# Kernel optimization log

Hardware: AMD Instinct MI355X
Metric: run time of the kernel (lower is better)

Reference implementation:

```python
import jax, jax.numpy as jnp
import numpy as np

N = 4096
HIDDEN = 256
NUM_HEADS = 8
HEAD_DIM = HIDDEN // NUM_HEADS
LN_EPS = 1e-3


def setup_inputs() -> dict:
    key = jax.random.key(0)
    ks = jax.random.split(key, 8)
    s = 1.0 / np.sqrt(HIDDEN)
    feat = jax.random.normal(ks[0], (N, HIDDEN), dtype=jnp.float32)
    Wq = jax.random.normal(ks[1], (HIDDEN, HIDDEN), dtype=jnp.float32) * s
    bq = jnp.zeros((HIDDEN,), dtype=jnp.float32)
    Wkv = jax.random.normal(ks[2], (HIDDEN, 2 * HIDDEN), dtype=jnp.float32) * s
    bkv = jnp.zeros((2 * HIDDEN,), dtype=jnp.float32)
    Weg = jax.random.normal(ks[3], (HIDDEN, 2 * NUM_HEADS), dtype=jnp.float32) * s
    beg = jnp.zeros((2 * NUM_HEADS,), dtype=jnp.float32)
    ln_g = jnp.ones((HIDDEN,), dtype=jnp.float32)
    ln_b = jnp.zeros((HIDDEN,), dtype=jnp.float32)
    return {"feat": feat, "Wq": Wq, "bq": bq, "Wkv": Wkv, "bkv": bkv,
            "Weg": Weg, "beg": beg, "ln_g": ln_g, "ln_b": ln_b}


def reference(feat, Wq, bq, Wkv, bkv, Weg, beg, ln_g, ln_b):
    n = feat.shape[0]
    # projections
    Q = feat @ Wq + bq                                  # [N, hidden]
    KV = feat @ Wkv + bkv                               # [N, 2*hidden]
    K, V = jnp.split(KV, 2, axis=-1)
    EG = feat @ Weg + beg                               # [N, 2*heads]
    E, G = jnp.split(EG, 2, axis=-1)                    # each [N, heads]
    # reshape to [N, head_dim, heads] (heads is the FAST axis, as in torch .view)
    Q = Q.reshape(n, HEAD_DIM, NUM_HEADS) * (HEAD_DIM ** -0.5)
    K = K.reshape(n, HEAD_DIM, NUM_HEADS)
    V = V.reshape(n, HEAD_DIM, NUM_HEADS)
    # all-pairs scores with per-j edge bias: [N, N, heads]
    H = jnp.einsum('idh,jdh->ijh', Q, K) + E[None, :, :]
    # softmax over i (axis 0), post-softmax sigmoid gate (per j, h)
    A = jax.nn.softmax(H, axis=0) * jax.nn.sigmoid(G)[None, :, :]
    Va = jnp.einsum('ijh,jdh->idh', A, V).reshape(n, HIDDEN)
    # layernorm eps=1e-3
    mu = jnp.mean(Va, axis=-1, keepdims=True)
    var = jnp.var(Va, axis=-1, keepdims=True)
    return (Va - mu) * jax.lax.rsqrt(var + LN_EPS) * ln_g + ln_b
```

## Files before the change

### kernel.cpp

```cpp
#include <hip/hip_runtime.h>
#include <hip/hip_bf16.h>

#define N 4096
#define HID 256
#define NH 8
#define HD 32
#define NC 784
#define CH 8
#define JSPAN (N / CH)

typedef __attribute__((ext_vector_type(8))) short short8;
typedef __attribute__((ext_vector_type(4))) short short4v;
typedef __attribute__((ext_vector_type(4))) float f32x4;
typedef __attribute__((ext_vector_type(2))) unsigned int uint2v;
typedef __attribute__((ext_vector_type(4))) unsigned int uint4v;

#define QSCALE 0.25503482f

static __device__ __forceinline__ unsigned short f2bf(float f) {
    union { float f; unsigned u; } v; v.f = f;
    unsigned r = v.u + 0x7fff + ((v.u >> 16) & 1);
    return (unsigned short)(r >> 16);
}
static __device__ __forceinline__ float bf2f(unsigned short u) {
    union { unsigned u; float f; } v; v.u = ((unsigned)u) << 16; return v.f;
}
static __device__ __forceinline__ unsigned packbf2(float a, float b) {
    __hip_bfloat162 t = __float22bfloat162_rn(make_float2(a, b));
    unsigned u; __builtin_memcpy(&u, &t, 4); return u;
}

__global__ void k_prep(const float* __restrict__ feat, const float* __restrict__ Wq,
                       const float* __restrict__ Wkv, const float* __restrict__ Weg,
                       const float* __restrict__ bq, const float* __restrict__ bkv,
                       const float* __restrict__ beg, unsigned short* __restrict__ featb,
                       unsigned short* __restrict__ WbT, float* __restrict__ bC,
                       float* __restrict__ colS) {
    int bx = blockIdx.x;
    if (bx < 1024) {
        int t = bx * 256 + threadIdx.x;
        float4 v = ((const float4*)feat)[t];
        short4v o;
        o[0] = (short)f2bf(v.x); o[1] = (short)f2bf(v.y);
        o[2] = (short)f2bf(v.z); o[3] = (short)f2bf(v.w);
        ((short4v*)featb)[t] = o;
    } else {
        int c = bx - 1024, k = threadIdx.x;
        float w, b;
        if (c < 256)      { w = Wq[k * 256 + c];          b = bq[c]; }
        else if (c < 768) { w = Wkv[k * 512 + (c - 256)]; b = bkv[c - 256]; }
        else              { w = Weg[k * 16 + (c - 768)];  b = beg[c - 768]; }
        WbT[c * 256 + k] = f2bf(w);
        if (k == 0) bC[c] = b;
        if (c < 128) colS[c * 256 + k] = 0.f;
    }
}

__global__ __launch_bounds__(256) void k_proj(const unsigned short* __restrict__ featb,
                                              const unsigned short* __restrict__ WbT,
                                              const float* __restrict__ bC,
                                              unsigned short* __restrict__ Qp,
                                              unsigned short* __restrict__ Kp,
                                              unsigned short* __restrict__ VpT,
                                              float* __restrict__ sigG) {
    int w = threadIdx.x >> 6, l = threadIdx.x & 63;
    int il = l & 15, g = l >> 4;
    int c0 = blockIdx.x * 16;
    int i0 = (blockIdx.y * 4 + w) * 16;
    const short8* Arow = (const short8*)(featb + (size_t)(i0 + il) * HID);
    const short8* Brow = (const short8*)(WbT + (size_t)(c0 + il) * HID);
    f32x4 acc = {0.f, 0.f, 0.f, 0.f};
#pragma unroll
    for (int k0 = 0; k0 < HID; k0 += 32) {
        short8 a = Arow[(k0 >> 3) + g];
        short8 b = Brow[(k0 >> 3) + g];
        acc = __builtin_amdgcn_mfma_f32_16x16x32_bf16(a, b, acc, 0, 0, 0);
    }
    int c = c0 + il;
    float bias = bC[c];
#pragma unroll
    for (int r = 0; r < 4; ++r) {
        int i = i0 + g * 4 + r;
        float val = acc[r] + bias;
        if (c < 256) {
            int h = c & 7, d = c >> 3;
            Qp[((size_t)h * N + i) * HD + d] = f2bf(val * QSCALE);
        } else if (c < 512) {
            int cc = c - 256, h = cc & 7, d = cc >> 3;
            Kp[((size_t)h * N + i) * HD + d] = f2bf(val);
        } else if (c < 768) {
            int cc = c - 512, h = cc & 7, d = cc >> 3;
            VpT[((size_t)h * HD + d) * N + i] = f2bf(val);
        } else {
            int cc = c - 768;
            if (cc >= 8) sigG[(size_t)(cc - 8) * N + i] = 1.f / (1.f + __expf(-val));
        }
    }
}

__global__ __launch_bounds__(256) void k_pass1(const unsigned short* __restrict__ Qp,
                                               const unsigned short* __restrict__ Kp,
                                               float* __restrict__ colS) {
    int w = threadIdx.x >> 6, l = threadIdx.x & 63;
    int il = l & 15, g = l >> 4;
    int h = blockIdx.y;
    int j0 = (blockIdx.x * 4 + w) * 64;
    const unsigned short* Kh = Kp + (size_t)h * N * HD;
    short8 Kf[4];
#pragma unroll
    for (int t = 0; t < 4; ++t)
        Kf[t] = *(const short8*)(Kh + (size_t)(j0 + 16 * t + il) * HD + g * 8);
    const unsigned short* Qh = Qp + (size_t)h * N * HD;
    f32x4 z = {0.f, 0.f, 0.f, 0.f};
    float s[4] = {0.f, 0.f, 0.f, 0.f};
    int ibeg = blockIdx.z * 512;
    short8 Qa = *(const short8*)(Qh + (size_t)(ibeg + il) * HD + g * 8);
    short8 Qb = *(const short8*)(Qh + (size_t)(ibeg + 16 + il) * HD + g * 8);
    for (int i0 = ibeg; i0 < ibeg + 512; i0 += 32) {
        short8 cQa = Qa, cQb = Qb;
        int in = i0 + 32;
        Qa = *(const short8*)(Qh + (size_t)(in + il) * HD + g * 8);
        Qb = *(const short8*)(Qh + (size_t)(in + 16 + il) * HD + g * 8);
#pragma unroll
        for (int t = 0; t < 4; ++t) {
            f32x4 Sa = __builtin_amdgcn_mfma_f32_16x16x32_bf16(cQa, Kf[t], z, 0, 0, 0);
            f32x4 Sb = __builtin_amdgcn_mfma_f32_16x16x32_bf16(cQb, Kf[t], z, 0, 0, 0);
            s[t] += ((__builtin_amdgcn_exp2f(Sa[0]) + __builtin_amdgcn_exp2f(Sa[1]))
                   + (__builtin_amdgcn_exp2f(Sa[2]) + __builtin_amdgcn_exp2f(Sa[3])))
                  + ((__builtin_amdgcn_exp2f(Sb[0]) + __builtin_amdgcn_exp2f(Sb[1]))
                   + (__builtin_amdgcn_exp2f(Sb[2]) + __builtin_amdgcn_exp2f(Sb[3])));
        }
    }
#pragma unroll
    for (int t = 0; t < 4; ++t) {
        s[t] += __shfl_xor(s[t], 16);
        s[t] += __shfl_xor(s[t], 32);
    }
    if (g == 0) {
#pragma unroll
        for (int t = 0; t < 4; ++t)
            atomicAdd(&colS[(size_t)h * N + j0 + 16 * t + il], s[t]);
    }
}

__global__ void k_vprep(unsigned short* __restrict__ VpT,
                        const float* __restrict__ sigG,
                        const float* __restrict__ colS) {
    int row = blockIdx.x >> 1;
    int j0 = ((blockIdx.x & 1) * 256 + threadIdx.x) * 8;
    int h = row >> 5;
    unsigned short* p = VpT + (size_t)row * N + j0;
    short8 v = *(short8*)p;
    const float* sg = sigG + (size_t)h * N + j0;
    const float* cs = colS + (size_t)h * N + j0;
    f32x4 sa = *(const f32x4*)sg, sb = *(const f32x4*)(sg + 4);
    f32x4 ca = *(const f32x4*)cs, cb = *(const f32x4*)(cs + 4);
    unsigned o[4];
    o[0] = packbf2(bf2f((unsigned short)v[0]) * sa[0] / ca[0],
                   bf2f((unsigned short)v[1]) * sa[1] / ca[1]);
    o[1] = packbf2(bf2f((unsigned short)v[2]) * sa[2] / ca[2],
                   bf2f((unsigned short)v[3]) * sa[3] / ca[3]);
    o[2] = packbf2(bf2f((unsigned short)v[4]) * sb[0] / cb[0],
                   bf2f((unsigned short)v[5]) * sb[1] / cb[1]);
    o[3] = packbf2(bf2f((unsigned short)v[6]) * sb[2] / cb[2],
                   bf2f((unsigned short)v[7]) * sb[3] / cb[3]);
    uint4v ov; ov[0] = o[0]; ov[1] = o[1]; ov[2] = o[2]; ov[3] = o[3];
    *(uint4v*)p = ov;
}

static __device__ __forceinline__ short8 frag_dance(f32x4 Sa, f32x4 Sb) {
    unsigned A0 = packbf2(__builtin_amdgcn_exp2f(Sa[0]), __builtin_amdgcn_exp2f(Sa[1]));
    unsigned A1 = packbf2(__builtin_amdgcn_exp2f(Sa[2]), __builtin_amdgcn_exp2f(Sa[3]));
    unsigned B0 = packbf2(__builtin_amdgcn_exp2f(Sb[0]), __builtin_amdgcn_exp2f(Sb[1]));
    unsigned B1 = packbf2(__builtin_amdgcn_exp2f(Sb[2]), __builtin_amdgcn_exp2f(Sb[3]));
    uint2v r1 = __builtin_amdgcn_permlane32_swap(A0, B0, false, false);
    uint2v r2 = __builtin_amdgcn_permlane16_swap(r1[0], r1[1], false, false);
    uint2v r3 = __builtin_amdgcn_permlane32_swap(A1, B1, false, false);
    uint2v r4 = __builtin_amdgcn_permlane16_swap(r3[0], r3[1], false, false);
    uint4v pu;
    pu[0] = r2[0]; pu[1] = r4[0]; pu[2] = r2[1]; pu[3] = r4[1];
    return __builtin_bit_cast(short8, pu);
}

__global__ __launch_bounds__(256) void k_pass2(const unsigned short* __restrict__ Qp,
                                               const unsigned short* __restrict__ Kp,
                                               const unsigned short* __restrict__ VpT,
                                               float* __restrict__ Vpart) {
    int w = threadIdx.x >> 6, l = threadIdx.x & 63;
    int il = l & 15, g = l >> 4;
    int h = blockIdx.y;
    int i0 = (blockIdx.x * 4 + w) * 64;
    int jbeg = blockIdx.z * JSPAN;
    const unsigned short* Qh = Qp + (size_t)h * N * HD;
    const unsigned short* Kh = Kp + ((size_t)h * N + jbeg) * HD;
    const unsigned short* Vh = VpT + (size_t)h * HD * N + jbeg;
    short8 Qf[4];
#pragma unroll
    for (int q = 0; q < 4; ++q)
        Qf[q] = *(const short8*)(Qh + (size_t)(i0 + q * 16 + il) * HD + g * 8);
    f32x4 z = {0.f, 0.f, 0.f, 0.f};
    f32x4 acc[4][2];
#pragma unroll
    for (int q = 0; q < 4; ++q) {
        acc[q][0] = z;
        acc[q][1] = z;
    }
    short8 K0 = *(const short8*)(Kh + (size_t)il * HD + g * 8);
    short8 K1 = *(const short8*)(Kh + (size_t)(16 + il) * HD + g * 8);
    short8 V0 = *(const short8*)(Vh + (size_t)il * N + g * 8);
    short8 V1 = *(const short8*)(Vh + (size_t)(16 + il) * N + g * 8);
    for (int jb = 0; jb < JSPAN; jb += 32) {
        short8 cK0 = K0, cK1 = K1, cV0 = V0, cV1 = V1;
        int jn = jb + 32;
        K0 = *(const short8*)(Kh + (size_t)(jn + il) * HD + g * 8);
        K1 = *(const short8*)(Kh + (size_t)(jn + 16 + il) * HD + g * 8);
        V0 = *(const short8*)(Vh + (size_t)il * N + jn + g * 8);
        V1 = *(const short8*)(Vh + (size_t)(16 + il) * N + jn + g * 8);
#pragma unroll
        for (int q = 0; q < 4; ++q) {
            f32x4 SA = __builtin_amdgcn_mfma_f32_16x16x32_bf16(cK0, Qf[q], z, 0, 0, 0);
            f32x4 SB = __builtin_amdgcn_mfma_f32_16x16x32_bf16(cK1, Qf[q], z, 0, 0, 0);
            short8 Pa = frag_dance(SA, SB);
            acc[q][0] = __builtin_amdgcn_mfma_f32_16x16x32_bf16(Pa, cV0, acc[q][0], 0, 0, 0);
            acc[q][1] = __builtin_amdgcn_mfma_f32_16x16x32_bf16(Pa, cV1, acc[q][1], 0, 0, 0);
        }
    }
    float* Vout = Vpart + (size_t)(blockIdx.z * NH + h) * N * HD;
#pragma unroll
    for (int q = 0; q < 4; ++q) {
#pragma unroll
        for (int r = 0; r < 4; ++r) {
            int ia = i0 + q * 16 + g * 4 + r;
            Vout[(size_t)ia * HD + il]      = acc[q][0][r];
            Vout[(size_t)ia * HD + 16 + il] = acc[q][1][r];
        }
    }
}

__global__ __launch_bounds__(256) void k_ln(const float* __restrict__ Vpart,
                                            const float* __restrict__ gam,
                                            const float* __restrict__ bet,
                                            float* __restrict__ out) {
    int w = threadIdx.x >> 6, l = threadIdx.x & 63;
    int i = blockIdx.x * 4 + w;
    int h = l >> 3, d0 = (l & 7) << 2;
    f32x4 x = {0.f, 0.f, 0.f, 0.f};
#pragma unroll
    for (int c = 0; c < CH; ++c) {
        f32x4 v = *(const f32x4*)(Vpart + ((size_t)(c * NH + h) * N + i) * HD + d0);
        x[0] += v[0]; x[1] += v[1]; x[2] += v[2]; x[3] += v[3];
    }
    float s1 = x[0] + x[1] + x[2] + x[3];
    float s2 = x[0] * x[0] + x[1] * x[1] + x[2] * x[2] + x[3] * x[3];
#pragma unroll
    for (int off = 1; off < 64; off <<= 1) {
        s1 += __shfl_xor(s1, off);
        s2 += __shfl_xor(s2, off);
    }
    float mu = s1 * (1.f / 256.f);
    float var = s2 * (1.f / 256.f) - mu * mu;
    float rs = rsqrtf(var + 1e-3f);
#pragma unroll
    for (int r = 0; r < 4; ++r) {
        int c = (d0 + r) * 8 + h;
        out[(size_t)i * HID + c] = (x[r] - mu) * rs * gam[c] + bet[c];
    }
}

extern "C" void kernel_launch(void* const* d_in, const int* in_sizes, int n_in,
                              void* d_out, int out_size, void* d_ws, size_t ws_size,
                              hipStream_t stream) {
    const float* feat = (const float*)d_in[0];
    const float* Wq   = (const float*)d_in[1];
    const float* bq   = (const float*)d_in[2];
    const float* Wkv  = (const float*)d_in[3];
    const float* bkv  = (const float*)d_in[4];
    const float* Weg  = (const float*)d_in[5];
    const float* beg  = (const float*)d_in[6];
    const float* ln_g = (const float*)d_in[7];
    const float* ln_b = (const float*)d_in[8];
    float* out = (float*)d_out;

    char* ws = (char*)d_ws;
    unsigned short* Qp    = (unsigned short*)(ws + 0);
    unsigned short* Kp    = (unsigned short*)(ws + (2u << 20));
    unsigned short* VpT   = (unsigned short*)(ws + (4u << 20));
    unsigned short* featb = (unsigned short*)(ws + (6u << 20));
    unsigned short* WbT   = (unsigned short*)(ws + (8u << 20));
    float* bC   = (float*)(ws + (8u << 20) + (512u << 10));
    float* sigG = (float*)(ws + (8u << 20) + (528u << 10));
    float* colS = (float*)(ws + (8u << 20) + (656u << 10));
    float* Vpart = (float*)(ws + (9u << 20));

    k_prep<<<dim3(1024 + NC), 256, 0, stream>>>(feat, Wq, Wkv, Weg, bq, bkv, beg,
                                                featb, WbT, bC, colS);
    k_proj<<<dim3(49, 64), 256, 0, stream>>>(featb, WbT, bC, Qp, Kp, VpT, sigG);
    k_pass1<<<dim3(16, NH, 8), 256, 0, stream>>>(Qp, Kp, colS);
    k_vprep<<<dim3(512), 256, 0, stream>>>(VpT, sigG, colS);
    k_pass2<<<dim3(16, NH, CH), 256, 0, stream>>>(Qp, Kp, VpT, Vpart);
    k_ln<<<dim3(1024), 256, 0, stream>>>(Vpart, ln_g, ln_b, out);
}
```

Measured before the change: 111.4 us.

## Split pass1/pass2 work finer, combine warp partials in LDS, store bf16 partials

Pass1 now gives each block half as many query rows and launches twice as many blocks along z. Pass2 now uses two-wave blocks: each wave covers half of a chunk's j-range for the same 64 query rows, and the two partials are summed through shared memory. The partial V outputs are written as bf16 instead of fp32, and the layernorm kernel reads them back as bf16. The aims are more parallel blocks and less partial-output traffic, at the cost of an extra barrier plus LDS round-trip and bf16 rounding of the partial sums.

```diff
diff --git a/kernel.cpp b/kernel.cpp
--- a/kernel.cpp
+++ b/kernel.cpp
@@ -113,10 +113,10 @@
     const unsigned short* Qh = Qp + (size_t)h * N * HD;
     f32x4 z = {0.f, 0.f, 0.f, 0.f};
     float s[4] = {0.f, 0.f, 0.f, 0.f};
-    int ibeg = blockIdx.z * 512;
+    int ibeg = blockIdx.z * 256;
     short8 Qa = *(const short8*)(Qh + (size_t)(ibeg + il) * HD + g * 8);
     short8 Qb = *(const short8*)(Qh + (size_t)(ibeg + 16 + il) * HD + g * 8);
-    for (int i0 = ibeg; i0 < ibeg + 512; i0 += 32) {
+    for (int i0 = ibeg; i0 < ibeg + 256; i0 += 32) {
         short8 cQa = Qa, cQb = Qb;
         int in = i0 + 32;
         Qa = *(const short8*)(Qh + (size_t)(in + il) * HD + g * 8);
@@ -182,15 +182,16 @@
     return __builtin_bit_cast(short8, pu);
 }
 
-__global__ __launch_bounds__(256) void k_pass2(const unsigned short* __restrict__ Qp,
+__global__ __launch_bounds__(128) void k_pass2(const unsigned short* __restrict__ Qp,
                                                const unsigned short* __restrict__ Kp,
                                                const unsigned short* __restrict__ VpT,
-                                               float* __restrict__ Vpart) {
+                                               unsigned short* __restrict__ Vpb) {
+    __shared__ __align__(16) float comb[64 * 36];
     int w = threadIdx.x >> 6, l = threadIdx.x & 63;
     int il = l & 15, g = l >> 4;
     int h = blockIdx.y;
-    int i0 = (blockIdx.x * 4 + w) * 64;
-    int jbeg = blockIdx.z * JSPAN;
+    int i0 = blockIdx.x * 64;
+    int jbeg = blockIdx.z * JSPAN + w * (JSPAN / 2);
     const unsigned short* Qh = Qp + (size_t)h * N * HD;
     const unsigned short* Kh = Kp + ((size_t)h * N + jbeg) * HD;
     const unsigned short* Vh = VpT + (size_t)h * HD * N + jbeg;
@@ -201,15 +202,12 @@
     f32x4 z = {0.f, 0.f, 0.f, 0.f};
     f32x4 acc[4][2];
 #pragma unroll
-    for (int q = 0; q < 4; ++q) {
-        acc[q][0] = z;
-        acc[q][1] = z;
-    }
+    for (int q = 0; q < 4; ++q) { acc[q][0] = z; acc[q][1] = z; }
     short8 K0 = *(const short8*)(Kh + (size_t)il * HD + g * 8);
     short8 K1 = *(const short8*)(Kh + (size_t)(16 + il) * HD + g * 8);
     short8 V0 = *(const short8*)(Vh + (size_t)il * N + g * 8);
     short8 V1 = *(const short8*)(Vh + (size_t)(16 + il) * N + g * 8);
-    for (int jb = 0; jb < JSPAN; jb += 32) {
+    for (int jb = 0; jb < JSPAN / 2; jb += 32) {
         short8 cK0 = K0, cK1 = K1, cV0 = V0, cV1 = V1;
         int jn = jb + 32;
         K0 = *(const short8*)(Kh + (size_t)(jn + il) * HD + g * 8);
@@ -225,19 +223,31 @@
             acc[q][1] = __builtin_amdgcn_mfma_f32_16x16x32_bf16(Pa, cV1, acc[q][1], 0, 0, 0);
         }
     }
-    float* Vout = Vpart + (size_t)(blockIdx.z * NH + h) * N * HD;
-#pragma unroll
-    for (int q = 0; q < 4; ++q) {
-#pragma unroll
-        for (int r = 0; r < 4; ++r) {
-            int ia = i0 + q * 16 + g * 4 + r;
-            Vout[(size_t)ia * HD + il]      = acc[q][0][r];
-            Vout[(size_t)ia * HD + 16 + il] = acc[q][1][r];
-        }
-    }
-}
-
-__global__ __launch_bounds__(256) void k_ln(const float* __restrict__ Vpart,
+    if (w == 1) {
+#pragma unroll
+        for (int q = 0; q < 4; ++q) {
+            *(f32x4*)(comb + l * 36 + q * 8)     = acc[q][0];
+            *(f32x4*)(comb + l * 36 + q * 8 + 4) = acc[q][1];
+        }
+    }
+    __syncthreads();
+    if (w == 0) {
+        unsigned short* Vout = Vpb + (size_t)(blockIdx.z * NH + h) * N * HD;
+#pragma unroll
+        for (int q = 0; q < 4; ++q) {
+            f32x4 o0 = *(const f32x4*)(comb + l * 36 + q * 8);
+            f32x4 o1 = *(const f32x4*)(comb + l * 36 + q * 8 + 4);
+#pragma unroll
+            for (int r = 0; r < 4; ++r) {
+                int ia = i0 + q * 16 + g * 4 + r;
+                Vout[(size_t)ia * HD + il]      = f2bf(acc[q][0][r] + o0[r]);
+                Vout[(size_t)ia * HD + 16 + il] = f2bf(acc[q][1][r] + o1[r]);
+            }
+        }
+    }
+}
+
+__global__ __launch_bounds__(256) void k_ln(const unsigned short* __restrict__ Vpb,
                                             const float* __restrict__ gam,
                                             const float* __restrict__ bet,
                                             float* __restrict__ out) {
@@ -247,8 +257,9 @@
     f32x4 x = {0.f, 0.f, 0.f, 0.f};
 #pragma unroll
     for (int c = 0; c < CH; ++c) {
-        f32x4 v = *(const f32x4*)(Vpart + ((size_t)(c * NH + h) * N + i) * HD + d0);
-        x[0] += v[0]; x[1] += v[1]; x[2] += v[2]; x[3] += v[3];
+        short4v v = *(const short4v*)(Vpb + ((size_t)(c * NH + h) * N + i) * HD + d0);
+        x[0] += bf2f((unsigned short)v[0]); x[1] += bf2f((unsigned short)v[1]);
+        x[2] += bf2f((unsigned short)v[2]); x[3] += bf2f((unsigned short)v[3]);
     }
     float s1 = x[0] + x[1] + x[2] + x[3];
     float s2 = x[0] * x[0] + x[1] * x[1] + x[2] * x[2] + x[3] * x[3];
@@ -290,13 +301,13 @@
     float* bC   = (float*)(ws + (8u << 20) + (512u << 10));
     float* sigG = (float*)(ws + (8u << 20) + (528u << 10));
     float* colS = (float*)(ws + (8u << 20) + (656u << 10));
-    float* Vpart = (float*)(ws + (9u << 20));
+    unsigned short* Vpb = (unsigned short*)(ws + (9u << 20));
 
     k_prep<<<dim3(1024 + NC), 256, 0, stream>>>(feat, Wq, Wkv, Weg, bq, bkv, beg,
                                                 featb, WbT, bC, colS);
     k_proj<<<dim3(49, 64), 256, 0, stream>>>(featb, WbT, bC, Qp, Kp, VpT, sigG);
-    k_pass1<<<dim3(16, NH, 8), 256, 0, stream>>>(Qp, Kp, colS);
+    k_pass1<<<dim3(16, NH, 16), 256, 0, stream>>>(Qp, Kp, colS);
     k_vprep<<<dim3(512), 256, 0, stream>>>(VpT, sigG, colS);
-    k_pass2<<<dim3(16, NH, CH), 256, 0, stream>>>(Qp, Kp, VpT, Vpart);
-    k_ln<<<dim3(1024), 256, 0, stream>>>(Vpart, ln_g, ln_b, out);
-}
+    k_pass2<<<dim3(64, NH, CH), 128, 0, stream>>>(Qp, Kp, VpT, Vpb);
+    k_ln<<<dim3(1024), 256, 0, stream>>>(Vpb, ln_g, ln_b, out);
+}
```

New measurement: 107.4 us. 1.04x faster.
